# Kernel tuning notes

Hardware: AMD Instinct MI355X
Metric: run time of the kernel (lower is better)

## Reference

```python
import jax, jax.numpy as jnp
import numpy as np

B, S, E, H = 2, 2048, 1024, 16
Dh = E // H
LN_EPS = 1e-5


def setup_inputs() -> dict:
    key = jax.random.key(0)
    ks = jax.random.split(key, 12)
    std = 1.0 / np.sqrt(E)
    inp = {
        "query": jax.random.normal(ks[0], (B, S, E), jnp.float32),
        "key":   jax.random.normal(ks[1], (B, S, E), jnp.float32),
        "value": jax.random.normal(ks[2], (B, S, E), jnp.float32),
        # True = masked. Causal mask so every row keeps >=1 valid entry.
        "mask": jnp.broadcast_to(jnp.triu(jnp.ones((S, S), bool), k=1), (B, S, S)),
        # per-head QKV projections, stacked: weight [H, Dh, E] (torch Linear layout), bias [H, Dh]
        "Wq_w": jax.random.uniform(ks[3], (H, Dh, E), jnp.float32, -std, std),
        "Wq_b": jax.random.uniform(ks[4], (H, Dh), jnp.float32, -std, std),
        "Wk_w": jax.random.uniform(ks[5], (H, Dh, E), jnp.float32, -std, std),
        "Wk_b": jax.random.uniform(ks[6], (H, Dh), jnp.float32, -std, std),
        "Wv_w": jax.random.uniform(ks[7], (H, Dh, E), jnp.float32, -std, std),
        "Wv_b": jax.random.uniform(ks[8], (H, Dh), jnp.float32, -std, std),
        # output projection [E, E] (torch layout: out = x @ W.T + b)
        "out_w": jax.random.uniform(ks[9], (E, E), jnp.float32, -std, std),
        "out_b": jax.random.uniform(ks[10], (E,), jnp.float32, -std, std),
        "ln_g": jnp.ones((E,), jnp.float32),
        "ln_b": jnp.zeros((E,), jnp.float32),
    }
    return inp


def reference(query, key, value, mask, Wq_w, Wq_b, Wk_w, Wk_b, Wv_w, Wv_b, out_w, out_b, ln_g, ln_b):
    # per-head projections (batched over heads): [B,S,E] x [H,Dh,E] -> [B,H,S,Dh]
    q = jnp.einsum('bse,hde->bhsd', query, Wq_w) + Wq_b[None, :, None, :]
    k = jnp.einsum('bse,hde->bhsd', key,   Wk_w) + Wk_b[None, :, None, :]
    v = jnp.einsum('bse,hde->bhsd', value, Wv_w) + Wv_b[None, :, None, :]
    scale = 1.0 / np.sqrt(Dh).astype(np.float32)
    scores = jnp.einsum('bhsd,bhtd->bhst', q, k) * scale  # [B,H,S,S]
    scores = jnp.where(mask[:, None, :, :], -jnp.inf, scores)
    probs = jax.nn.softmax(scores, axis=-1)  # dropout p=0 (eval)
    ctx = jnp.einsum('bhst,bhtd->bhsd', probs, v)  # [B,H,S,Dh]
    att = ctx.transpose(0, 2, 1, 3).reshape(query.shape[0], query.shape[1], -1)  # concat heads [B,S,E]
    proj = att @ out_w.T + out_b  # dropout p=0
    x = query + proj  # residual
    mu = jnp.mean(x, axis=-1, keepdims=True)
    var = jnp.mean(jnp.square(x - mu), axis=-1, keepdims=True)
    return (x - mu) * jax.lax.rsqrt(var + LN_EPS) * ln_g + ln_b
```

## Files before the change

kernel.cpp:

```cpp
#include <hip/hip_runtime.h>
#include <stdint.h>

#define B_ 2
#define S_ 2048
#define E_ 1024
#define H_ 16
#define DH 64
#define M_TOT (B_*S_)

typedef short s16x8 __attribute__((ext_vector_type(8)));
typedef float f32x4 __attribute__((ext_vector_type(4)));
typedef unsigned int u32;
typedef unsigned short u16;

union V8 { uint4 u; s16x8 v; };

__device__ __forceinline__ u32 fbits(float f){ union{float f;u32 i;}x; x.f=f; return x.i; }
__device__ __forceinline__ u32 prround(float f){ return fbits(f)+0x8000u; }
__device__ __forceinline__ u16 f2bf(float f){ return (u16)(prround(f)>>16); }
__device__ __forceinline__ u32 permpack(u32 hi,u32 lo){ return __builtin_amdgcn_perm(hi,lo,0x07060302u); }
__device__ __forceinline__ uint4 pack8r(const float4 a, const float4 b){
    uint4 p;
    p.x = permpack(prround(a.y),prround(a.x));
    p.y = permpack(prround(a.w),prround(a.z));
    p.z = permpack(prround(b.y),prround(b.x));
    p.w = permpack(prround(b.w),prround(b.z));
    return p;
}
__device__ __forceinline__ float exp2_fast(float x){ float r; asm("v_exp_f32 %0, %1":"=v"(r):"v"(x)); return r; }

typedef const __attribute__((address_space(1))) u32* gas_t;
typedef __attribute__((address_space(3))) u32* las_t;
#define GLDS16(gp, lp) __builtin_amdgcn_global_load_lds((gas_t)(gp), (las_t)(lp), 16, 0, 0)

#define MFMA16(a,b,c) __builtin_amdgcn_mfma_f32_16x16x32_bf16((a),(b),(c),0,0,0)

__global__ __launch_bounds__(256) void cvtw(
    const float* __restrict__ w0, const float* __restrict__ w1, const float* __restrict__ w2,
    u16* __restrict__ dst, int n4)
{
    const int z = blockIdx.y;
    const float* s = (z==0)?w0:(z==1)?w1:w2;
    u16* d = dst + (size_t)z*E_*E_;
    int i = blockIdx.x*256 + threadIdx.x;
    const int stride = gridDim.x*256;
    for (; i<n4; i+=stride){
        float4 v = ((const float4*)s)[i];
        uint2 p;
        p.x = permpack(prround(v.y),prround(v.x));
        p.y = permpack(prround(v.w),prround(v.z));
        ((uint2*)d)[i] = p;
    }
}
__global__ __launch_bounds__(256) void cvt1(
    const float* __restrict__ s, u16* __restrict__ d, int n4)
{
    int i = blockIdx.x*256 + threadIdx.x;
    const int stride = gridDim.x*256;
    for (; i<n4; i+=stride){
        float4 v = ((const float4*)s)[i];
        uint2 p;
        p.x = permpack(prround(v.y),prround(v.x));
        p.y = permpack(prround(v.w),prround(v.z));
        ((uint2*)d)[i] = p;
    }
}

__global__ __launch_bounds__(256,3) void qkv128(
    const float* __restrict__ xq, const float* __restrict__ xk, const float* __restrict__ xv,
    const u16* __restrict__ Wb,
    const float* __restrict__ bq, const float* __restrict__ bk, const float* __restrict__ bv,
    u16* __restrict__ oq, u16* __restrict__ ok_, u16* __restrict__ ovt)
{
    const int bid = blockIdx.x;
    const int c = bid & 7;
    const int tdec = bid >> 3;
    const int n = tdec & 7;
    const int g = ((tdec >> 3) << 3) + c;
    const int m = g & 31, z = g >> 5;

    const float* X = (z==0)?xq:(z==1)?xk:xv;
    const u16* W = Wb + (size_t)z*E_*E_;
    const float* bia = (z==0)?bq:(z==1)?bk:bv;
    const float scale = (z==0)? 0.125f*1.44269504f : 1.0f;

    __shared__ __align__(16) u16 As[3][128*32];
    __shared__ __align__(16) u16 Bs[3][128*32];

    const int tid = threadIdx.x;
    const int wid = tid>>6, lane = tid&63;
    const int lrow = lane&15, quad = lane>>4;
    const int mb = m*128, nb = n*128;
    const int wm = (wid>>1)*64, wn = (wid&1)*64;
    const int srow = lane>>2, skq = lane&3;
    const int arow = wid*32 + (lane>>1);
    const int akh  = lane&1;

    f32x4 acc[4][4] = {};
    const float* Xb = X + (size_t)mb*E_;
    const u16*  Wn = W + (size_t)nb*E_;
    const float* Xrow = Xb + (size_t)arow*E_ + akh*16;

    float4 ar[4];
    auto issueA = [&](int kt){
        const int k0 = kt*32;
#pragma unroll
        for (int i=0;i<4;i++) ar[i] = *(const float4*)(Xrow + k0 + i*4);
    };
    auto writeA = [&](u16* Ad){
        const int g0 = akh*2;
        const int sw = arow&3;
        const uint4 w0 = pack8r(ar[0], ar[1]);
        const uint4 w1 = pack8r(ar[2], ar[3]);
        *(uint4*)&Ad[arow*32 + (((g0  )^sw)<<3)] = w0;
        *(uint4*)&Ad[arow*32 + (((g0+1)^sw)<<3)] = w1;
    };
    auto stageB = [&](u16* Bd, int kt){
        const int k0 = kt*32;
#pragma unroll
        for (int i=0;i<2;i++){
            const int rb = wid*32 + i*16;
            GLDS16(Wn + (size_t)(rb+srow)*E_ + k0 + ((skq^(srow&3))<<3), Bd + rb*32);
        }
    };

    issueA(0); stageB(Bs[0], 0); writeA(As[0]);
    issueA(1); stageB(Bs[1], 1); writeA(As[1]);

    int tc = 0, tn = 2;
    for (int kt=0; kt<32; ++kt){
        const int ts = (kt+2 < 32) ? kt+2 : 31;
        asm volatile("s_waitcnt vmcnt(2) lgkmcnt(0)" ::: "memory");
        __builtin_amdgcn_s_barrier();
        __builtin_amdgcn_sched_barrier(0);

        const u16* Ad = As[tc];
        const u16* Bd = Bs[tc];
        const int sw = lrow&3;
        s16x8 a0 = *(const s16x8*)&Ad[(wm+ 0+lrow)*32 + ((quad^sw)<<3)];
        s16x8 a1 = *(const s16x8*)&Ad[(wm+16+lrow)*32 + ((quad^sw)<<3)];
        s16x8 b0 = *(const s16x8*)&Bd[(wn+ 0+lrow)*32 + ((quad^sw)<<3)];
        s16x8 b1 = *(const s16x8*)&Bd[(wn+16+lrow)*32 + ((quad^sw)<<3)];
        s16x8 b2 = *(const s16x8*)&Bd[(wn+32+lrow)*32 + ((quad^sw)<<3)];
        s16x8 b3 = *(const s16x8*)&Bd[(wn+48+lrow)*32 + ((quad^sw)<<3)];
        issueA(ts);
        __builtin_amdgcn_sched_barrier(0);
        stageB(Bs[tn], ts);
        __builtin_amdgcn_s_setprio(1);
        acc[0][0] = MFMA16(a0, b0, acc[0][0]);
        acc[0][1] = MFMA16(a0, b1, acc[0][1]);
        acc[0][2] = MFMA16(a0, b2, acc[0][2]);
        acc[0][3] = MFMA16(a0, b3, acc[0][3]);
        acc[1][0] = MFMA16(a1, b0, acc[1][0]);
        acc[1][1] = MFMA16(a1, b1, acc[1][1]);
        acc[1][2] = MFMA16(a1, b2, acc[1][2]);
        acc[1][3] = MFMA16(a1, b3, acc[1][3]);
        __builtin_amdgcn_s_setprio(0);
        s16x8 a2 = *(const s16x8*)&Ad[(wm+32+lrow)*32 + ((quad^sw)<<3)];
        s16x8 a3 = *(const s16x8*)&Ad[(wm+48+lrow)*32 + ((quad^sw)<<3)];
        writeA(As[tn]);
        __builtin_amdgcn_s_setprio(1);
        acc[2][0] = MFMA16(a2, b0, acc[2][0]);
        acc[2][1] = MFMA16(a2, b1, acc[2][1]);
        acc[2][2] = MFMA16(a2, b2, acc[2][2]);
        acc[2][3] = MFMA16(a2, b3, acc[2][3]);
        acc[3][0] = MFMA16(a3, b0, acc[3][0]);
        acc[3][1] = MFMA16(a3, b1, acc[3][1]);
        acc[3][2] = MFMA16(a3, b2, acc[3][2]);
        acc[3][3] = MFMA16(a3, b3, acc[3][3]);
        __builtin_amdgcn_s_setprio(0);
        tc = (tc+1==3)?0:tc+1;
        tn = (tn+1==3)?0:tn+1;
    }
    asm volatile("s_waitcnt vmcnt(0)" ::: "memory");

    if (z < 2){
        u16* O = (z==0)?oq:ok_;
#pragma unroll
        for (int ci=0;ci<4;ci++){
            const int nn = nb+wn+ci*16+lrow;
            const float bval = bia[nn];
            const int h = nn>>6, d = nn&63;
#pragma unroll
            for (int mi=0;mi<4;mi++){
#pragma unroll
                for (int r=0;r<4;r++){
                    const int mm = mb+wm+mi*16+quad*4+r;
                    const int bb = mm>>11, s = mm&(S_-1);
                    O[(((size_t)(bb*H_+h))*S_+s)*DH + d] = f2bf((acc[mi][ci][r]+bval)*scale);
                }
            }
        }
    } else {
#pragma unroll
        for (int ci=0;ci<4;ci++){
            const int nn = nb+wn+ci*16+lrow;
            const float bval = bia[nn];
            const int h = nn>>6, d = nn&63;
#pragma unroll
            for (int mi=0;mi<4;mi++){
                const int m0 = mb+wm+mi*16+quad*4;
                const int bb = m0>>11, s0 = m0&(S_-1);
                uint2 pk;
                pk.x = permpack(prround(acc[mi][ci][1]+bval), prround(acc[mi][ci][0]+bval));
                pk.y = permpack(prround(acc[mi][ci][3]+bval), prround(acc[mi][ci][2]+bval));
                *(uint2*)&ovt[(((size_t)(bb*H_+h))*DH + d)*S_ + s0] = pk;
            }
        }
    }
}

__global__ __launch_bounds__(256) void attn(
    const u16* __restrict__ q_ws, const u16* __restrict__ k_ws,
    const u16* __restrict__ vt_ws, u16* __restrict__ att)
{
    const int bid = blockIdx.x;
    const int c8 = bid & 7;
    const int t = bid >> 3;
    const int p = t & 15;
    const int bh = ((t >> 4) << 3) + c8;
    const int b = bh>>4, h = bh&15;

    const u16* Qb = q_ws + (size_t)bh*S_*DH;
    const u16* Kb = k_ws + (size_t)bh*S_*DH;
    const u16* VT = vt_ws + (size_t)bh*DH*S_;

    __shared__ __align__(16) u16 Ks0[64*64];
    __shared__ __align__(16) u16 Ks1[64*64];
    __shared__ __align__(16) u16 Vt0[64*64];
    __shared__ __align__(16) u16 Vt1[64*64];
    __shared__ __align__(16) u16 Ps[4][16*64];

    const int tid = threadIdx.x;
    const int wid = tid>>6, lane = tid&63;
    const int lrow = lane&15, quad = lane>>4;
    u16* Pw = Ps[wid];

    const int srw = lane>>3;
    const int scs = lane&7;
    const int sgc = scs ^ srw;

    auto stageKV = [&](u16* Kd, u16* Vd, int t0){
#pragma unroll
        for (int g2=0; g2<2; g2++){
            const int rg = wid*16 + g2*8 + srw;
            GLDS16(Kb + (size_t)(t0+rg)*DH + (sgc<<3), Kd + (wid*16+g2*8)*64);
            GLDS16(VT + (size_t)rg*S_ + t0 + (sgc<<3), Vd + (wid*16+g2*8)*64);
        }
    };

    for (int ph=0; ph<2; ph++){
        const int qi = ph ? (31-p) : p;
        const int qb = qi<<6;

        s16x8 qf[2];
#pragma unroll
        for (int ch=0;ch<2;ch++)
            qf[ch] = *(const s16x8*)&Qb[(size_t)(qb+wid*16+lrow)*DH + ch*32 + quad*8];

        f32x4 o[4] = {};
        float l_lane = 0.f;
        const int qglob = qb + wid*16 + lrow;
        const int ntile = qi + 1;

        auto computeTile = [&](const u16* Kd, const u16* Vd, int t0, bool diag){
            f32x4 st[4] = {};
#pragma unroll
            for (int tt=0;tt<4;tt++){
                const int tr = tt*16+lrow;
#pragma unroll
                for (int ch=0;ch<2;ch++){
                    const int slot = (ch*4+quad) ^ (lrow&7);
                    const s16x8 kf = *(const s16x8*)&Kd[tr*64 + slot*8];
                    st[tt] = __builtin_amdgcn_mfma_f32_16x16x32_bf16(kf, qf[ch], st[tt],0,0,0);
                }
            }
            if (diag){
#pragma unroll
                for (int tt=0;tt<4;tt++){
                    const int tg = t0 + tt*16 + quad*4;
#pragma unroll
                    for (int r=0;r<4;r++)
                        if (tg + r > qglob) st[tt][r] = -1e30f;
                }
            }
#pragma unroll
            for (int tt=0;tt<4;tt++){
                const float p0 = exp2_fast(st[tt][0]);
                const float p1 = exp2_fast(st[tt][1]);
                const float p2 = exp2_fast(st[tt][2]);
                const float p3 = exp2_fast(st[tt][3]);
                l_lane += (p0+p1)+(p2+p3);
                const int tc = tt*2 + (quad>>1);
                const int ts = tc ^ (lrow&7);
                const int a0 = lrow*64 + ts*8 + (quad&1)*4;
                *(u32*)&Pw[a0]   = permpack(prround(p1),prround(p0));
                *(u32*)&Pw[a0+2] = permpack(prround(p3),prround(p2));
            }
            s16x8 pb[2];
#pragma unroll
            for (int ch=0;ch<2;ch++){
                const int slot = (ch*4+quad) ^ (lrow&7);
                pb[ch] = *(const s16x8*)&Pw[lrow*64 + slot*8];
            }
#pragma unroll
            for (int cc=0;cc<4;cc++){
                const int vr = cc*16+lrow;
#pragma unroll
                for (int ch=0;ch<2;ch++){
                    const int slot = (ch*4+quad) ^ (lrow&7);
                    const s16x8 vf = *(const s16x8*)&Vd[vr*64 + slot*8];
                    o[cc] = __builtin_amdgcn_mfma_f32_16x16x32_bf16(vf, pb[ch], o[cc],0,0,0);
                }
            }
        };

        __syncthreads();
        stageKV(Ks0, Vt0, 0);
        for (int ti=0; ; ti+=2){
            __syncthreads();
            if (ti+1 < ntile) stageKV(Ks1, Vt1, (ti+1)<<6);
            computeTile(Ks0, Vt0, ti<<6, ti==ntile-1);
            if (ti+1 >= ntile) break;
            __syncthreads();
            if (ti+2 < ntile) stageKV(Ks0, Vt0, (ti+2)<<6);
            computeTile(Ks1, Vt1, (ti+1)<<6, ti+1==ntile-1);
            if (ti+2 >= ntile) break;
        }

        float s = l_lane;
        s += __shfl_xor(s, 16, 64);
        s += __shfl_xor(s, 32, 64);
        const float rl = 1.0f/s;

#pragma unroll
        for (int cc=0;cc<4;cc++){
            uint2 pk;
            pk.x = permpack(prround(o[cc][1]*rl), prround(o[cc][0]*rl));
            pk.y = permpack(prround(o[cc][3]*rl), prround(o[cc][2]*rl));
            *(uint2*)&att[(size_t)(b*S_ + qglob)*E_ + h*DH + cc*16 + quad*4] = pk;
        }
    }
}

__global__ __launch_bounds__(256) void oproj128(
    const u16* __restrict__ A, const u16* __restrict__ W, const float* __restrict__ bias,
    const float* __restrict__ resid, float* __restrict__ out)
{
    const int bid = blockIdx.x;
    const int c = bid & 7;
    const int tdec = bid >> 3;
    const int n = tdec & 15;
    const int m = ((tdec >> 4) << 3) + c;

    __shared__ __align__(16) u16 As[3][128*32];
    __shared__ __align__(16) u16 Bs[3][64*32];

    const int tid = threadIdx.x;
    const int wid = tid>>6, lane = tid&63;
    const int lrow = lane&15, quad = lane>>4;
    const int mb = m*128, nb = n*64;
    const int srow = lane>>2, skq = lane&3;

    f32x4 acc[2][4] = {};
    const u16* Ab = A + (size_t)mb*E_;
    const u16* Wn = W + (size_t)nb*E_;

    auto stage = [&](u16* Ad, u16* Bd, int kt){
        const int k0 = kt*32;
        const int kc = (skq^(srow&3))<<3;
#pragma unroll
        for (int i=0;i<2;i++){
            const int rb = wid*32 + i*16;
            GLDS16(Ab + (size_t)(rb+srow)*E_ + k0 + kc, Ad + rb*32);
        }
        GLDS16(Wn + (size_t)(wid*16+srow)*E_ + k0 + kc, Bd + (wid*16)*32);
    };

    stage(As[0], Bs[0], 0);
    stage(As[1], Bs[1], 1);

    int tc = 0, tn = 2;
    for (int kt=0; kt<32; ++kt){
        const int ts = (kt+2 < 32) ? kt+2 : 31;
        asm volatile("s_waitcnt vmcnt(3) lgkmcnt(0)" ::: "memory");
        __builtin_amdgcn_s_barrier();
        __builtin_amdgcn_sched_barrier(0);

        const u16* Ad = As[tc];
        const u16* Bd = Bs[tc];
        const int sw = lrow&3;
        s16x8 a0 = *(const s16x8*)&Ad[(wid*32+ 0+lrow)*32 + ((quad^sw)<<3)];
        s16x8 a1 = *(const s16x8*)&Ad[(wid*32+16+lrow)*32 + ((quad^sw)<<3)];
        s16x8 b0 = *(const s16x8*)&Bd[( 0+lrow)*32 + ((quad^sw)<<3)];
        s16x8 b1 = *(const s16x8*)&Bd[(16+lrow)*32 + ((quad^sw)<<3)];
        s16x8 b2 = *(const s16x8*)&Bd[(32+lrow)*32 + ((quad^sw)<<3)];
        s16x8 b3 = *(const s16x8*)&Bd[(48+lrow)*32 + ((quad^sw)<<3)];
        stage(As[tn], Bs[tn], ts);
        __builtin_amdgcn_s_setprio(1);
        acc[0][0] = MFMA16(a0, b0, acc[0][0]);
        acc[0][1] = MFMA16(a0, b1, acc[0][1]);
        acc[0][2] = MFMA16(a0, b2, acc[0][2]);
        acc[0][3] = MFMA16(a0, b3, acc[0][3]);
        acc[1][0] = MFMA16(a1, b0, acc[1][0]);
        acc[1][1] = MFMA16(a1, b1, acc[1][1]);
        acc[1][2] = MFMA16(a1, b2, acc[1][2]);
        acc[1][3] = MFMA16(a1, b3, acc[1][3]);
        __builtin_amdgcn_s_setprio(0);
        tc = (tc+1==3)?0:tc+1;
        tn = (tn+1==3)?0:tn+1;
    }
    asm volatile("s_waitcnt vmcnt(0)" ::: "memory");

#pragma unroll
    for (int ci=0;ci<4;ci++){
        const int nn = nb+ci*16+lrow;
        const float bval = bias[nn];
#pragma unroll
        for (int mi=0;mi<2;mi++){
#pragma unroll
            for (int r=0;r<4;r++){
                const int mm = mb+wid*32+mi*16+quad*4+r;
                out[(size_t)mm*E_+nn] = acc[mi][ci][r] + bval + resid[(size_t)mm*E_+nn];
            }
        }
    }
}

__global__ __launch_bounds__(256) void ln_k(
    const float* __restrict__ xin, const float* __restrict__ lg,
    const float* __restrict__ lb, float* __restrict__ out)
{
    const int row = blockIdx.x;
    const int tid = threadIdx.x;
    const int wid = tid>>6, lane = tid&63;
    const float* xr = xin + (size_t)row*E_;

    float x[4];
    float s = 0.f;
#pragma unroll
    for (int i=0;i<4;i++){ const int e = i*256+tid; x[i] = xr[e]; s += x[i]; }
    __shared__ float red[8];
#pragma unroll
    for (int off=32; off>0; off>>=1) s += __shfl_xor(s, off, 64);
    if (lane==0) red[wid] = s;
    __syncthreads();
    const float mu = (red[0]+red[1]+red[2]+red[3]) * (1.f/E_);

    float v = 0.f;
#pragma unroll
    for (int i=0;i<4;i++){ const float d = x[i]-mu; v += d*d; }
#pragma unroll
    for (int off=32; off>0; off>>=1) v += __shfl_xor(v, off, 64);
    if (lane==0) red[wid+4] = v;
    __syncthreads();
    const float var = (red[4]+red[5]+red[6]+red[7]) * (1.f/E_);
    const float rs = rsqrtf(var + 1e-5f);

#pragma unroll
    for (int i=0;i<4;i++){
        const int e = i*256+tid;
        out[(size_t)row*E_+e] = (x[i]-mu)*rs*lg[e] + lb[e];
    }
}

extern "C" void kernel_launch(void* const* d_in, const int* in_sizes, int n_in,
                              void* d_out, int out_size, void* d_ws, size_t ws_size,
                              hipStream_t stream) {
    const float* q_in = (const float*)d_in[0];
    const float* k_in = (const float*)d_in[1];
    const float* v_in = (const float*)d_in[2];
    const float* wq = (const float*)d_in[4];
    const float* bq = (const float*)d_in[5];
    const float* wk = (const float*)d_in[6];
    const float* bk = (const float*)d_in[7];
    const float* wv = (const float*)d_in[8];
    const float* bv = (const float*)d_in[9];
    const float* ow = (const float*)d_in[10];
    const float* ob = (const float*)d_in[11];
    const float* lg = (const float*)d_in[12];
    const float* lb = (const float*)d_in[13];
    float* out = (float*)d_out;

    char* ws = (char*)d_ws;
    const size_t MB = (size_t)1<<20;
    u16* q_ws  = (u16*)(ws);
    u16* k_ws  = (u16*)(ws +  8*MB);
    u16* vt_ws = (u16*)(ws + 16*MB);
    u16* att   = (u16*)(ws + 24*MB);
    u16* Wbf   = (u16*)(ws + 24*MB);
    u16* owbf  = (u16*)(ws + 16*MB);
    float* proj = (float*)ws;

    cvtw<<<dim3(512,3), 256, 0, stream>>>(wq, wk, wv, Wbf, (E_*E_)/4);
    qkv128<<<dim3(768), 256, 0, stream>>>(
        q_in, k_in, v_in, Wbf, bq, bk, bv, q_ws, k_ws, vt_ws);
    attn<<<dim3(512), 256, 0, stream>>>(q_ws, k_ws, vt_ws, att);
    cvt1<<<dim3(1024), 256, 0, stream>>>(ow, owbf, (E_*E_)/4);
    oproj128<<<dim3(512), 256, 0, stream>>>(att, owbf, ob, q_in, proj);
    ln_k<<<dim3(M_TOT), 256, 0, stream>>>(proj, lg, lb, out);
}
```

Baseline: 253.7 us.

## Double-buffer A-operand registers to deepen global load pipeline in QKV GEMM

The QKV projection main loop now keeps two register sets for the fp32 A tile, so each tile's global loads are issued a full iteration before that tile is packed into shared memory. The wait is relaxed from vmcnt(2) to vmcnt(6), and the loop is manually unrolled by two to alternate the register sets. All A and B fragments are read from LDS up front rather than split around the A write. The aim is to hide global load latency for the fp32 activations, at the cost of more live registers, which may lower occupancy.

After: 249.2 us. About the same (-1.8%).

```diff
diff --git a/kernel.cpp b/kernel.cpp
--- a/kernel.cpp
+++ b/kernel.cpp
@@ -95,26 +95,17 @@
     const int srow = lane>>2, skq = lane&3;
     const int arow = wid*32 + (lane>>1);
     const int akh  = lane&1;
+    const int ag0  = akh*2;
+    const int asw  = arow&3;
 
     f32x4 acc[4][4] = {};
     const float* Xb = X + (size_t)mb*E_;
     const u16*  Wn = W + (size_t)nb*E_;
     const float* Xrow = Xb + (size_t)arow*E_ + akh*16;
 
-    float4 ar[4];
-    auto issueA = [&](int kt){
-        const int k0 = kt*32;
-#pragma unroll
-        for (int i=0;i<4;i++) ar[i] = *(const float4*)(Xrow + k0 + i*4);
-    };
-    auto writeA = [&](u16* Ad){
-        const int g0 = akh*2;
-        const int sw = arow&3;
-        const uint4 w0 = pack8r(ar[0], ar[1]);
-        const uint4 w1 = pack8r(ar[2], ar[3]);
-        *(uint4*)&Ad[arow*32 + (((g0  )^sw)<<3)] = w0;
-        *(uint4*)&Ad[arow*32 + (((g0+1)^sw)<<3)] = w1;
-    };
+    float4 arA0, arA1, arA2, arA3;
+    float4 arB0, arB1, arB2, arB3;
+
     auto stageB = [&](u16* Bd, int kt){
         const int k0 = kt*32;
 #pragma unroll
@@ -124,55 +115,87 @@
         }
     };
 
-    issueA(0); stageB(Bs[0], 0); writeA(As[0]);
-    issueA(1); stageB(Bs[1], 1); writeA(As[1]);
-
-    int tc = 0, tn = 2;
-    for (int kt=0; kt<32; ++kt){
-        const int ts = (kt+2 < 32) ? kt+2 : 31;
-        asm volatile("s_waitcnt vmcnt(2) lgkmcnt(0)" ::: "memory");
-        __builtin_amdgcn_s_barrier();
-        __builtin_amdgcn_sched_barrier(0);
-
-        const u16* Ad = As[tc];
-        const u16* Bd = Bs[tc];
-        const int sw = lrow&3;
-        s16x8 a0 = *(const s16x8*)&Ad[(wm+ 0+lrow)*32 + ((quad^sw)<<3)];
-        s16x8 a1 = *(const s16x8*)&Ad[(wm+16+lrow)*32 + ((quad^sw)<<3)];
-        s16x8 b0 = *(const s16x8*)&Bd[(wn+ 0+lrow)*32 + ((quad^sw)<<3)];
-        s16x8 b1 = *(const s16x8*)&Bd[(wn+16+lrow)*32 + ((quad^sw)<<3)];
-        s16x8 b2 = *(const s16x8*)&Bd[(wn+32+lrow)*32 + ((quad^sw)<<3)];
-        s16x8 b3 = *(const s16x8*)&Bd[(wn+48+lrow)*32 + ((quad^sw)<<3)];
-        issueA(ts);
-        __builtin_amdgcn_sched_barrier(0);
-        stageB(Bs[tn], ts);
-        __builtin_amdgcn_s_setprio(1);
-        acc[0][0] = MFMA16(a0, b0, acc[0][0]);
-        acc[0][1] = MFMA16(a0, b1, acc[0][1]);
-        acc[0][2] = MFMA16(a0, b2, acc[0][2]);
-        acc[0][3] = MFMA16(a0, b3, acc[0][3]);
-        acc[1][0] = MFMA16(a1, b0, acc[1][0]);
-        acc[1][1] = MFMA16(a1, b1, acc[1][1]);
-        acc[1][2] = MFMA16(a1, b2, acc[1][2]);
-        acc[1][3] = MFMA16(a1, b3, acc[1][3]);
-        __builtin_amdgcn_s_setprio(0);
-        s16x8 a2 = *(const s16x8*)&Ad[(wm+32+lrow)*32 + ((quad^sw)<<3)];
-        s16x8 a3 = *(const s16x8*)&Ad[(wm+48+lrow)*32 + ((quad^sw)<<3)];
-        writeA(As[tn]);
-        __builtin_amdgcn_s_setprio(1);
-        acc[2][0] = MFMA16(a2, b0, acc[2][0]);
-        acc[2][1] = MFMA16(a2, b1, acc[2][1]);
-        acc[2][2] = MFMA16(a2, b2, acc[2][2]);
-        acc[2][3] = MFMA16(a2, b3, acc[2][3]);
-        acc[3][0] = MFMA16(a3, b0, acc[3][0]);
-        acc[3][1] = MFMA16(a3, b1, acc[3][1]);
-        acc[3][2] = MFMA16(a3, b2, acc[3][2]);
-        acc[3][3] = MFMA16(a3, b3, acc[3][3]);
-        __builtin_amdgcn_s_setprio(0);
+#define QKV_ISSUEA(KT, AR) do {                                   \
+        const float* xp_ = Xrow + ((KT)<<5);                      \
+        AR##0 = *(const float4*)(xp_    );                        \
+        AR##1 = *(const float4*)(xp_ + 4);                        \
+        AR##2 = *(const float4*)(xp_ + 8);                        \
+        AR##3 = *(const float4*)(xp_ +12);                        \
+    } while(0)
+
+#define QKV_WRITEA(AD, AR) do {                                   \
+        const uint4 w0_ = pack8r(AR##0, AR##1);                   \
+        const uint4 w1_ = pack8r(AR##2, AR##3);                   \
+        *(uint4*)&(AD)[arow*32 + (((ag0  )^asw)<<3)] = w0_;       \
+        *(uint4*)&(AD)[arow*32 + (((ag0+1)^asw)<<3)] = w1_;       \
+    } while(0)
+
+#define QKV_ITER(KT, TC, ARC, ARN) do {                                       \
+        const int ts_ = ((KT)+2 < 32) ? (KT)+2 : 31;                          \
+        const int tw_ = ((TC)+1==3)?0:(TC)+1;                                 \
+        const int tn_ = (tw_+1==3)?0:tw_+1;                                   \
+        const u16* Ad_ = As[TC];                                              \
+        const u16* Bd_ = Bs[TC];                                              \
+        asm volatile("s_waitcnt vmcnt(6) lgkmcnt(0)" ::: "memory");           \
+        __builtin_amdgcn_s_barrier();                                         \
+        __builtin_amdgcn_sched_barrier(0);                                    \
+        const int fq_ = (quad^(lrow&3))<<3;                                   \
+        s16x8 a0 = *(const s16x8*)&Ad_[(wm+ 0+lrow)*32 + fq_];                \
+        s16x8 a1 = *(const s16x8*)&Ad_[(wm+16+lrow)*32 + fq_];                \
+        s16x8 a2 = *(const s16x8*)&Ad_[(wm+32+lrow)*32 + fq_];                \
+        s16x8 a3 = *(const s16x8*)&Ad_[(wm+48+lrow)*32 + fq_];                \
+        s16x8 b0 = *(const s16x8*)&Bd_[(wn+ 0+lrow)*32 + fq_];                \
+        s16x8 b1 = *(const s16x8*)&Bd_[(wn+16+lrow)*32 + fq_];                \
+        s16x8 b2 = *(const s16x8*)&Bd_[(wn+32+lrow)*32 + fq_];                \
+        s16x8 b3 = *(const s16x8*)&Bd_[(wn+48+lrow)*32 + fq_];                \
+        __builtin_amdgcn_sched_barrier(0);                                    \
+        QKV_ISSUEA(ts_, ARN);                                                 \
+        __builtin_amdgcn_sched_barrier(0);                                    \
+        stageB(Bs[tn_], ts_);                                                 \
+        __builtin_amdgcn_sched_barrier(0);                                    \
+        __builtin_amdgcn_s_setprio(1);                                        \
+        acc[0][0] = MFMA16(a0, b0, acc[0][0]);                                \
+        acc[0][1] = MFMA16(a0, b1, acc[0][1]);                                \
+        acc[0][2] = MFMA16(a0, b2, acc[0][2]);                                \
+        acc[0][3] = MFMA16(a0, b3, acc[0][3]);                                \
+        acc[1][0] = MFMA16(a1, b0, acc[1][0]);                                \
+        acc[1][1] = MFMA16(a1, b1, acc[1][1]);                                \
+        acc[1][2] = MFMA16(a1, b2, acc[1][2]);                                \
+        acc[1][3] = MFMA16(a1, b3, acc[1][3]);                                \
+        __builtin_amdgcn_s_setprio(0);                                        \
+        QKV_WRITEA(As[tw_], ARC);                                             \
+        __builtin_amdgcn_s_setprio(1);                                        \
+        acc[2][0] = MFMA16(a2, b0, acc[2][0]);                                \
+        acc[2][1] = MFMA16(a2, b1, acc[2][1]);                                \
+        acc[2][2] = MFMA16(a2, b2, acc[2][2]);                                \
+        acc[2][3] = MFMA16(a2, b3, acc[2][3]);                                \
+        acc[3][0] = MFMA16(a3, b0, acc[3][0]);                                \
+        acc[3][1] = MFMA16(a3, b1, acc[3][1]);                                \
+        acc[3][2] = MFMA16(a3, b2, acc[3][2]);                                \
+        acc[3][3] = MFMA16(a3, b3, acc[3][3]);                                \
+        __builtin_amdgcn_s_setprio(0);                                        \
+    } while(0)
+
+    QKV_ISSUEA(0, arA);
+    stageB(Bs[0], 0);
+    QKV_WRITEA(As[0], arA);
+    QKV_ISSUEA(1, arA);
+    stageB(Bs[1], 1);
+
+    int tc = 0;
+#pragma unroll 1
+    for (int k2=0; k2<16; ++k2){
+        const int kt0 = k2*2;
+        QKV_ITER(kt0,   tc, arA, arB);
         tc = (tc+1==3)?0:tc+1;
-        tn = (tn+1==3)?0:tn+1;
-    }
-    asm volatile("s_waitcnt vmcnt(0)" ::: "memory");
+        QKV_ITER(kt0+1, tc, arB, arA);
+        tc = (tc+1==3)?0:tc+1;
+    }
+    asm volatile("s_waitcnt vmcnt(0) lgkmcnt(0)" ::: "memory");
+
+#undef QKV_ITER
+#undef QKV_WRITEA
+#undef QKV_ISSUEA
 
     if (z < 2){
         u16* O = (z==0)?oq:ok_;
```
